# Performance work log

Hardware: AMD Instinct MI355X
Metric: run time of the kernel (lower is better)

The kernel has to match this reference:

```python
import jax, jax.numpy as jnp
import numpy as np

B, S, IN, OUT = 8, 4096, 1024, 1024


def setup_inputs() -> dict:
    key = jax.random.key(0)
    k1, k2, k3, k4, k5 = jax.random.split(key, 5)
    x = jax.random.normal(k1, (B, S, IN), dtype=jnp.float32)
    # pre-quantized int8 weight buffer [out, in]
    weight = jax.random.randint(k2, (OUT, IN), -127, 128, dtype=jnp.int32).astype(jnp.int8)
    bias = jax.random.normal(k3, (OUT,), dtype=jnp.float32) * 0.1
    # per-channel weight clip values (>0)
    w_clip_val = jax.random.uniform(k4, (OUT,), minval=0.5, maxval=2.0, dtype=jnp.float32)
    # smoothquant per-input-channel activation scaling factors (>0)
    smoothquant_scale = jax.random.uniform(k5, (IN,), minval=0.5, maxval=2.0, dtype=jnp.float32)
    return {"x": x, "weight": weight, "bias": bias,
            "w_clip_val": w_clip_val, "smoothquant_scale": smoothquant_scale}


def reference(x, weight, bias, w_clip_val, smoothquant_scale):
    # i8i8_aiu semantics for weight_quant_type='per_channel',
    # activ_quant_type='per_token' (symmetric -> zero_shift == 0), smoothquant=True.
    # 1) smoothquant: scale activations prior to quantization
    xs = x / smoothquant_scale                                   # [B,S,IN]
    # 2) per-token symmetric int8 quantization of activations
    a_scale = jnp.max(jnp.abs(xs), axis=-1, keepdims=True) / 127.0  # [B,S,1]
    a_scale = jnp.maximum(a_scale, 1e-8)
    x_int = jnp.round(jnp.clip(xs / a_scale, -127.0, 127.0)).astype(jnp.int8)
    acc = jax.lax.dot_general(x_int, weight,
                              dimension_numbers=(((2,), (1,)), ((), ())),
                              preferred_element_type=jnp.int32)
    # 4) fused dequant (per-token act scale * per-channel weight scale) + bias
    w_scale = w_clip_val / 127.0                                 # [OUT]
    return acc.astype(jnp.float32) * a_scale * w_scale + bias
```

## Files before the change

kernel.cpp:

```cpp
#include <hip/hip_runtime.h>
#include <stdint.h>

#define T_TOK 32768
#define NIN   1024
#define NOUT  1024

typedef int   v4i  __attribute__((ext_vector_type(4)));
typedef int   v16i __attribute__((ext_vector_type(16)));
typedef float v4f  __attribute__((ext_vector_type(4)));

#define MFMA_I8(a, b, c) __builtin_amdgcn_mfma_i32_32x32x32_i8(a, b, c, 0, 0, 0)

__device__ __forceinline__ void gload_lds16(const void* g, void* l) {
  __builtin_amdgcn_global_load_lds(
      (const __attribute__((address_space(1))) unsigned int*)g,
      (__attribute__((address_space(3))) unsigned int*)l, 16, 0, 0);
}


__global__ __launch_bounds__(256) void repack_w_frag(const int* __restrict__ w,
                                                     uint32_t* __restrict__ wf) {
  const int gid  = blockIdx.x * 256 + threadIdx.x;
  const int lane = gid & 63;
  const int ks   = (gid >> 6) & 31;
  const int nt   = gid >> 11;
  const int n    = nt * 32 + (lane & 31);
  const int kb   = ks * 32 + (lane >> 5) * 16;
  const int* src = w + (size_t)n * NIN + kb;
  uint32_t d[4];
#pragma unroll
  for (int q = 0; q < 4; ++q) {
    const int4 v = ((const int4*)src)[q];
    d[q] = (uint32_t)(v.x & 0xff) | ((uint32_t)(v.y & 0xff) << 8) |
           ((uint32_t)(v.z & 0xff) << 16) | ((uint32_t)(v.w & 0xff) << 24);
  }
  ((uint4*)wf)[gid] = make_uint4(d[0], d[1], d[2], d[3]);
}

__global__ __launch_bounds__(512) void quant2(const float* __restrict__ x,
                                              const float* __restrict__ sq,
                                              uint32_t* __restrict__ afw,
                                              float* __restrict__ asc) {
  __shared__ __align__(16) uint8_t Af[32 * NIN];

  const int tid  = threadIdx.x;
  const int lane = tid & 63;
  const int w    = tid >> 6;
  const int t0   = blockIdx.x * 32;

  {
    const v4f* sq4 = (const v4f*)sq;
    v4f rs[4];
#pragma unroll
    for (int j = 0; j < 4; ++j) {
      const v4f s = sq4[j * 64 + lane];
      rs[j].x = __builtin_amdgcn_rcpf(s.x);
      rs[j].y = __builtin_amdgcn_rcpf(s.y);
      rs[j].z = __builtin_amdgcn_rcpf(s.z);
      rs[j].w = __builtin_amdgcn_rcpf(s.w);
    }
#pragma unroll
    for (int i = 0; i < 4; ++i) {
      const int tl = w * 4 + i;
      const v4f* xr = (const v4f*)(x + (size_t)(t0 + tl) * NIN);
      v4f v[4];
      float m = 0.f;
#pragma unroll
      for (int j = 0; j < 4; ++j) {
        v4f a = __builtin_nontemporal_load(&xr[j * 64 + lane]);
        a.x *= rs[j].x; a.y *= rs[j].y; a.z *= rs[j].z; a.w *= rs[j].w;
        v[j] = a;
        m = fmaxf(m, fmaxf(fmaxf(fabsf(a.x), fabsf(a.y)),
                           fmaxf(fabsf(a.z), fabsf(a.w))));
      }
#pragma unroll
      for (int off = 1; off < 64; off <<= 1) m = fmaxf(m, __shfl_xor(m, off));
      const float as = fmaxf(m * (1.f / 127.f), 1e-8f);
      if (lane == 0) asc[t0 + tl] = as;
      const float ia = __builtin_amdgcn_rcpf(as);
#pragma unroll
      for (int j = 0; j < 4; ++j) {
        const int q0 = (int)rintf(fminf(fmaxf(v[j].x * ia, -127.f), 127.f));
        const int q1 = (int)rintf(fminf(fmaxf(v[j].y * ia, -127.f), 127.f));
        const int q2 = (int)rintf(fminf(fmaxf(v[j].z * ia, -127.f), 127.f));
        const int q3 = (int)rintf(fminf(fmaxf(v[j].w * ia, -127.f), 127.f));
        const uint32_t d = (uint32_t)(q0 & 0xff) | ((uint32_t)(q1 & 0xff) << 8) |
                           ((uint32_t)(q2 & 0xff) << 16) | ((uint32_t)(q3 & 0xff) << 24);
        const int di   = j * 64 + lane;
        const int ksw  = di >> 3;
        const int h    = (di >> 2) & 1;
        const int slot = ((tl ^ (ksw & 7)) & 31) + 32 * h;
        *(uint32_t*)(&Af[(ksw * 64 + slot) * 16 + (di & 3) * 4]) = d;
      }
    }
  }
  __syncthreads();

  v4i* dst = (v4i*)afw + (size_t)blockIdx.x * 2048;
#pragma unroll
  for (int p = 0; p < 4; ++p) {
    const int cg = p * 512 + tid;
    const int ks = cg >> 6;
    const int lc = (cg & ~31) | ((cg ^ (ks & 7)) & 31);
    __builtin_nontemporal_store(*(const v4i*)(&Af[lc * 16]), &dst[cg]);
  }
}

__global__ __launch_bounds__(256, 2) void gemm2(
    const uint8_t* __restrict__ af,
    const uint8_t* __restrict__ wf,
    const float* __restrict__ asc,
    const float* __restrict__ wclip,
    const float* __restrict__ bias,
    float* __restrict__ out)
{
  __shared__ __align__(16) uint8_t As[64 * 1024];

  const int g   = blockIdx.x;
  const int xcd = g & 7;
  const int j   = g >> 3;
  const int T   = xcd * 32 + (j >> 2);
  const int nb  = j & 3;

  const int tid  = threadIdx.x;
  const int lane = tid & 63;
  const int w    = tid >> 6;

  const uint8_t* Abase = af + ((size_t)(T * 4) << 15);
  const uint8_t* Bb    = wf + ((size_t)(nb * 8 + w * 2) << 15) + lane * 16;

  auto stage_half = [&](int h) {
#pragma unroll
    for (int p = 0; p < 16; ++p) {
      const int off = p * 4096 + tid * 16;
      const int mt  = off >> 14;
      const int inr = off & 16383;
      gload_lds16(Abase + mt * 32768 + h * 16384 + inr, As + off);
    }
  };
  auto ldA = [&](int mt, int ksl) -> v4i {
    return *(const v4i*)(As + (((mt * 16 + ksl) * 64) + lane) * 16);
  };
  auto ldB = [&](int ks, int ntl) -> v4i {
    return *(const v4i*)(Bb + ntl * 32768 + ks * 1024);
  };

  v16i acc[4][2] = {};
  v4i Bae[2], Bao[2];

  stage_half(0);
  Bae[0] = ldB(0, 0); Bae[1] = ldB(0, 1);
  Bao[0] = ldB(1, 0); Bao[1] = ldB(1, 1);
  __syncthreads();

#define STEP(KSL, BREG, KN)                                                  \
  do {                                                                       \
    v4i a[4];                                                                \
    _Pragma("unroll") for (int mt = 0; mt < 4; ++mt) a[mt] = ldA(mt, (KSL)); \
    __builtin_amdgcn_s_setprio(1);                                           \
    _Pragma("unroll") for (int mt = 0; mt < 4; ++mt) {                       \
      acc[mt][0] = MFMA_I8(a[mt], BREG[0], acc[mt][0]);                      \
      acc[mt][1] = MFMA_I8(a[mt], BREG[1], acc[mt][1]);                      \
    }                                                                        \
    __builtin_amdgcn_s_setprio(0);                                           \
    if ((KN) < 32) { BREG[0] = ldB((KN), 0); BREG[1] = ldB((KN), 1); }       \
  } while (0)

#pragma unroll
  for (int h = 0; h < 2; ++h) {
    if (h == 1) {
      __syncthreads();
      stage_half(1);
      __syncthreads();
    }
#pragma unroll
    for (int kp = 0; kp < 16; kp += 2) {
      const int ks = h * 16 + kp;
      STEP(kp,     Bae, ks + 2);
      STEP(kp + 1, Bao, ks + 3);
    }
  }
#undef STEP

  const int hr = 4 * (lane >> 5);
#pragma unroll
  for (int mt = 0; mt < 4; ++mt) {
    const int t0 = T * 128 + mt * 32;
    float ascv[16];
#pragma unroll
    for (int reg = 0; reg < 16; ++reg)
      ascv[reg] = asc[t0 + (reg & 3) + 8 * (reg >> 2) + hr];
#pragma unroll
    for (int ntl = 0; ntl < 2; ++ntl) {
      const int n = nb * 256 + (w * 2 + ntl) * 32 + (lane & 31);
      const float wsc = wclip[n] * (1.f / 127.f);
      const float bs  = bias[n];
#pragma unroll
      for (int reg = 0; reg < 16; ++reg) {
        const int r = t0 + (reg & 3) + 8 * (reg >> 2) + hr;
        __builtin_nontemporal_store(
            (float)acc[mt][ntl][reg] * ascv[reg] * wsc + bs,
            &out[(size_t)r * NOUT + n]);
      }
    }
  }
}

extern "C" void kernel_launch(void* const* d_in, const int* in_sizes, int n_in,
                              void* d_out, int out_size, void* d_ws, size_t ws_size,
                              hipStream_t stream) {
  const float* x      = (const float*)d_in[0];
  const int*   weight = (const int*)d_in[1];
  const float* bias   = (const float*)d_in[2];
  const float* wclip  = (const float*)d_in[3];
  const float* sq     = (const float*)d_in[4];
  float* out = (float*)d_out;

  uint8_t* ws = (uint8_t*)d_ws;
  uint32_t* wfrag = (uint32_t*)ws;
  uint32_t* afrag = (uint32_t*)(ws + (1u << 20));
  float*    ascp  = (float*)(ws + (1u << 20) + ((size_t)T_TOK * NIN));

  repack_w_frag<<<(NOUT * NIN / 16) / 256, 256, 0, stream>>>(weight, wfrag);
  quant2<<<T_TOK / 32, 512, 0, stream>>>(x, sq, afrag, ascp);
  gemm2<<<1024, 256, 0, stream>>>((const uint8_t*)afrag, (const uint8_t*)wfrag,
                                  ascp, wclip, bias, out);
}
```

Before: 93.37 us.

## Split GEMM block tile across eight waves in a 2x4 grid

The GEMM block grows from 256 to 512 threads, and its 128x256 output tile is split into a 2x4 wave grid. Each wave now holds a 2x2 set of 32x32 accumulators instead of 4x2, which halves accumulator registers per wave and doubles the number of waves available to hide latency. The LDS A staging load is spread over more threads, so each thread issues fewer loads. In exchange, each wave now loads its own B fragments from global memory, so B traffic per block doubles, and launch bounds of 512 threads with 4 blocks may be hard to meet given the 64KB LDS per block.

```diff
diff --git a/kernel.cpp b/kernel.cpp
--- a/kernel.cpp
+++ b/kernel.cpp
@@ -106,7 +106,7 @@
   }
 }
 
-__global__ __launch_bounds__(256, 2) void gemm2(
+__global__ __launch_bounds__(512, 4) void gemm3(
     const uint8_t* __restrict__ af,
     const uint8_t* __restrict__ wf,
     const float* __restrict__ asc,
@@ -120,86 +120,86 @@
   const int xcd = g & 7;
   const int j   = g >> 3;
   const int T   = xcd * 32 + (j >> 2);
-  const int nb  = j & 3;
+  const int nq  = j & 3;
 
   const int tid  = threadIdx.x;
   const int lane = tid & 63;
   const int w    = tid >> 6;
+  const int wr   = w >> 2;
+  const int wc   = w & 3;
 
   const uint8_t* Abase = af + ((size_t)(T * 4) << 15);
-  const uint8_t* Bb    = wf + ((size_t)(nb * 8 + w * 2) << 15) + lane * 16;
+  const uint8_t* Bb = wf + ((size_t)(nq * 8 + wc * 2) << 15) + (size_t)lane * 16;
 
   auto stage_half = [&](int h) {
 #pragma unroll
-    for (int p = 0; p < 16; ++p) {
-      const int off = p * 4096 + tid * 16;
+    for (int p = 0; p < 8; ++p) {
+      const int off = p * 8192 + tid * 16;
       const int mt  = off >> 14;
       const int inr = off & 16383;
       gload_lds16(Abase + mt * 32768 + h * 16384 + inr, As + off);
     }
   };
-  auto ldA = [&](int mt, int ksl) -> v4i {
-    return *(const v4i*)(As + (((mt * 16 + ksl) * 64) + lane) * 16);
+  auto ldA = [&](int i, int ksl) -> v4i {
+    return *(const v4i*)(As + (wr * 2 + i) * 16384 + ksl * 1024 + lane * 16);
   };
-  auto ldB = [&](int ks, int ntl) -> v4i {
-    return *(const v4i*)(Bb + ntl * 32768 + ks * 1024);
+  auto ldB = [&](int ks, int i) -> v4i {
+    return *(const v4i*)(Bb + i * 32768 + ks * 1024);
   };
 
-  v16i acc[4][2] = {};
-  v4i Bae[2], Bao[2];
+  v16i acc[2][2] = {};
+  v4i Ba[2], Bo[2];
 
   stage_half(0);
-  Bae[0] = ldB(0, 0); Bae[1] = ldB(0, 1);
-  Bao[0] = ldB(1, 0); Bao[1] = ldB(1, 1);
-  __syncthreads();
-
-#define STEP(KSL, BREG, KN)                                                  \
+  Ba[0] = ldB(0, 0); Ba[1] = ldB(0, 1);
+  Bo[0] = ldB(1, 0); Bo[1] = ldB(1, 1);
+  __syncthreads();
+
+#define KSTEP(BR, KSL, KN)                                                   \
   do {                                                                       \
-    v4i a[4];                                                                \
-    _Pragma("unroll") for (int mt = 0; mt < 4; ++mt) a[mt] = ldA(mt, (KSL)); \
+    const v4i a0 = ldA(0, (KSL)), a1 = ldA(1, (KSL));                        \
     __builtin_amdgcn_s_setprio(1);                                           \
-    _Pragma("unroll") for (int mt = 0; mt < 4; ++mt) {                       \
-      acc[mt][0] = MFMA_I8(a[mt], BREG[0], acc[mt][0]);                      \
-      acc[mt][1] = MFMA_I8(a[mt], BREG[1], acc[mt][1]);                      \
-    }                                                                        \
+    acc[0][0] = MFMA_I8(a0, BR[0], acc[0][0]);                               \
+    acc[0][1] = MFMA_I8(a0, BR[1], acc[0][1]);                               \
+    acc[1][0] = MFMA_I8(a1, BR[0], acc[1][0]);                               \
+    acc[1][1] = MFMA_I8(a1, BR[1], acc[1][1]);                               \
     __builtin_amdgcn_s_setprio(0);                                           \
-    if ((KN) < 32) { BREG[0] = ldB((KN), 0); BREG[1] = ldB((KN), 1); }       \
+    if ((KN) < 32) { BR[0] = ldB((KN), 0); BR[1] = ldB((KN), 1); }           \
   } while (0)
 
 #pragma unroll
-  for (int h = 0; h < 2; ++h) {
-    if (h == 1) {
-      __syncthreads();
-      stage_half(1);
-      __syncthreads();
-    }
-#pragma unroll
-    for (int kp = 0; kp < 16; kp += 2) {
-      const int ks = h * 16 + kp;
-      STEP(kp,     Bae, ks + 2);
-      STEP(kp + 1, Bao, ks + 3);
-    }
-  }
-#undef STEP
+  for (int kp = 0; kp < 16; kp += 2) {
+    KSTEP(Ba, kp,     kp + 2);
+    KSTEP(Bo, kp + 1, kp + 3);
+  }
+  __syncthreads();
+  stage_half(1);
+  __syncthreads();
+#pragma unroll
+  for (int kp = 0; kp < 16; kp += 2) {
+    KSTEP(Ba, kp,     16 + kp + 2);
+    KSTEP(Bo, kp + 1, 16 + kp + 3);
+  }
+#undef KSTEP
 
   const int hr = 4 * (lane >> 5);
 #pragma unroll
-  for (int mt = 0; mt < 4; ++mt) {
-    const int t0 = T * 128 + mt * 32;
+  for (int i = 0; i < 2; ++i) {
+    const int t0 = T * 128 + (wr * 2 + i) * 32;
     float ascv[16];
 #pragma unroll
     for (int reg = 0; reg < 16; ++reg)
       ascv[reg] = asc[t0 + (reg & 3) + 8 * (reg >> 2) + hr];
 #pragma unroll
-    for (int ntl = 0; ntl < 2; ++ntl) {
-      const int n = nb * 256 + (w * 2 + ntl) * 32 + (lane & 31);
+    for (int jn = 0; jn < 2; ++jn) {
+      const int n = nq * 256 + wc * 64 + jn * 32 + (lane & 31);
       const float wsc = wclip[n] * (1.f / 127.f);
       const float bs  = bias[n];
 #pragma unroll
       for (int reg = 0; reg < 16; ++reg) {
         const int r = t0 + (reg & 3) + 8 * (reg >> 2) + hr;
         __builtin_nontemporal_store(
-            (float)acc[mt][ntl][reg] * ascv[reg] * wsc + bs,
+            (float)acc[i][jn][reg] * ascv[reg] * wsc + bs,
             &out[(size_t)r * NOUT + n]);
       }
     }
@@ -223,6 +223,6 @@
 
   repack_w_frag<<<(NOUT * NIN / 16) / 256, 256, 0, stream>>>(weight, wfrag);
   quant2<<<T_TOK / 32, 512, 0, stream>>>(x, sq, afrag, ascp);
-  gemm2<<<1024, 256, 0, stream>>>((const uint8_t*)afrag, (const uint8_t*)wfrag,
+  gemm3<<<1024, 512, 0, stream>>>((const uint8_t*)afrag, (const uint8_t*)wfrag,
                                   ascp, wclip, bias, out);
 }
```

After: 91.96 us. No clear change (-1.5%).
